# Optimization experiments

Hardware: AMD Instinct MI355X
Metric: run time of the kernel (lower is better)

The kernel has to match this reference:

```python
import jax, jax.numpy as jnp
import numpy as np

# NF4 codebook (bitsandbytes NormalFloat4 quantiles)
NF4_TABLE = jnp.array([
    -1.0, -0.6961928009986877, -0.5250730514526367, -0.39491748809814453,
    -0.28444138169288635, -0.18477343022823334, -0.09105003625154495, 0.0,
    0.07958029955625534, 0.16093020141124725, 0.24611230194568634,
    0.33791524171829224, 0.44070982933044434, 0.5626170039176941,
    0.7229568362236023, 1.0], dtype=jnp.float32)

BLOCK = 64  # bitsandbytes default quantization blocksize


def setup_inputs() -> dict:
    key = jax.random.key(0)
    ks = jax.random.split(key, 6)
    in_f, out_f, rank, n_tok = 4096, 4096, 16, 8192
    x = jax.random.normal(ks[0], (n_tok, in_f), dtype=jnp.float32)
    q_codes = jax.random.randint(ks[1], (out_f, in_f), 0, 16, dtype=jnp.int32)
    absmax = jax.random.uniform(ks[2], (out_f, in_f // BLOCK), dtype=jnp.float32) * 0.1 + 1e-3
    bias = jax.random.normal(ks[3], (out_f,), dtype=jnp.float32) * 0.02
    # kaiming-uniform-ish init for lora_down; lora_up nonzero for a meaningful test
    lora_down_w = jax.random.normal(ks[4], (rank, in_f), dtype=jnp.float32) * (1.0 / np.sqrt(in_f))
    lora_up_w = jax.random.normal(ks[5], (out_f, rank), dtype=jnp.float32) * 0.02
    alpha = jnp.array(16.0, dtype=jnp.float32)
    return {"x": x, "absmax": absmax, "bias": bias, "lora_down_w": lora_down_w,
            "lora_up_w": lora_up_w, "alpha": alpha, "q_codes": q_codes}


def reference(x, absmax, bias, lora_down_w, lora_up_w, alpha, q_codes):
    rank = lora_down_w.shape[0]
    # dequantize NF4 base weight: code lookup * per-block absmax scale
    w = NF4_TABLE[q_codes] * jnp.repeat(absmax, BLOCK, axis=1)  # [out, in]
    base = x @ w.T + bias                                       # [n_tok, out]
    # LoRA path: down [rank,in], up [out,rank], scaled by alpha/rank
    lora = (x @ lora_down_w.T) @ lora_up_w.T                    # [n_tok, out]
    return base + lora * (alpha / rank)
```

## Files before the change

### kernel.cpp

```cpp
#include <hip/hip_runtime.h>

#define IN_F 4096
#define OUT_F 4096
#define RANK 16
#define NTOK 8192
#define KP 4160
#define BK 64
#define NT (KP / BK)
#define BM 256
#define BN 256

typedef __bf16 bf16x8 __attribute__((ext_vector_type(8)));
typedef float f32x4 __attribute__((ext_vector_type(4)));

__device__ __forceinline__ unsigned short f2bf(float f) {
  unsigned int u = __float_as_uint(f);
  u += 0x7fffu + ((u >> 16) & 1u);
  return (unsigned short)(u >> 16);
}

__device__ __forceinline__ void async_ld16(const void* g, void* l) {
  __builtin_amdgcn_global_load_lds(
      (const __attribute__((address_space(1))) unsigned int*)g,
      (__attribute__((address_space(3))) unsigned int*)l, 16, 0, 0);
}

__device__ const float NF4_TAB[16] = {
    -1.0f, -0.6961928009986877f, -0.5250730514526367f, -0.39491748809814453f,
    -0.28444138169288635f, -0.18477343022823334f, -0.09105003625154495f, 0.0f,
    0.07958029955625534f, 0.16093020141124725f, 0.24611230194568634f,
    0.33791524171829224f, 0.44070982933044434f, 0.5626170039176941f,
    0.7229568362236023f, 1.0f};

__global__ __launch_bounds__(256) void k_prep_a(
    const float* __restrict__ x, const float* __restrict__ ldw,
    unsigned short* __restrict__ Ap) {
  const int tid = threadIdx.x;
  const int lane = tid & 63;
  const int w = tid >> 6;
  const int m0 = blockIdx.x * 4;

  float acc[4][4];
#pragma unroll
  for (int i = 0; i < 4; ++i)
#pragma unroll
    for (int rl = 0; rl < 4; ++rl) acc[i][rl] = 0.f;

  for (int c = 0; c < 16; ++c) {
    const int k0 = (c * 64 + lane) * 4;
    float4 xv[4];
#pragma unroll
    for (int i = 0; i < 4; ++i) {
      xv[i] = *(const float4*)&x[(size_t)(m0 + i) * IN_F + k0];
      if (w == i) {
        ushort4 s;
        s.x = f2bf(xv[i].x); s.y = f2bf(xv[i].y);
        s.z = f2bf(xv[i].z); s.w = f2bf(xv[i].w);
        *(ushort4*)&Ap[(size_t)(m0 + i) * KP + k0] = s;
      }
    }
#pragma unroll
    for (int rl = 0; rl < 4; ++rl) {
      float4 lv = *(const float4*)&ldw[(size_t)(w * 4 + rl) * IN_F + k0];
#pragma unroll
      for (int i = 0; i < 4; ++i)
        acc[i][rl] += xv[i].x * lv.x + xv[i].y * lv.y + xv[i].z * lv.z +
                      xv[i].w * lv.w;
    }
  }
#pragma unroll
  for (int i = 0; i < 4; ++i)
#pragma unroll
    for (int rl = 0; rl < 4; ++rl) {
      float v = acc[i][rl];
#pragma unroll
      for (int m = 1; m < 64; m <<= 1) v += __shfl_xor(v, m, 64);
      acc[i][rl] = v;
    }
  __shared__ float red[4][16];
  if (lane == 0) {
#pragma unroll
    for (int i = 0; i < 4; ++i)
#pragma unroll
      for (int rl = 0; rl < 4; ++rl) red[i][w * 4 + rl] = acc[i][rl];
  }
  __syncthreads();
  if (tid < 64) {
    Ap[(size_t)(m0 + (tid >> 4)) * KP + IN_F + (tid & 15)] =
        f2bf(red[tid >> 4][tid & 15]);
  } else {
    const int t2 = tid - 64;
    if (t2 < 192)
      Ap[(size_t)(m0 + t2 / 48) * KP + IN_F + 16 + (t2 % 48)] = 0;
  }
}

__global__ __launch_bounds__(256) void k_prep_b(
    const int* __restrict__ q, const float* __restrict__ amax,
    const float* __restrict__ luw, const float* __restrict__ alpha,
    unsigned short* __restrict__ Bp) {
  __shared__ float tab[16];
  const int tid = threadIdx.x;
  const int n = blockIdx.x;
  if (tid < 16) tab[tid] = NF4_TAB[tid];
  __syncthreads();
#pragma unroll
  for (int c = 0; c < 4; ++c) {
    const int k0 = (tid + 256 * c) * 4;
    int4 qv = *(const int4*)&q[(size_t)n * IN_F + k0];
    float am = amax[n * (IN_F / 64) + (k0 >> 6)];
    ushort4 s;
    s.x = f2bf(tab[qv.x] * am);
    s.y = f2bf(tab[qv.y] * am);
    s.z = f2bf(tab[qv.z] * am);
    s.w = f2bf(tab[qv.w] * am);
    *(ushort4*)&Bp[(size_t)n * KP + k0] = s;
  }
  if (tid < RANK) {
    float sc = alpha[0] * (1.0f / RANK);
    Bp[(size_t)n * KP + IN_F + tid] = f2bf(luw[n * RANK + tid] * sc);
  } else if (tid < 64) {
    Bp[(size_t)n * KP + IN_F + tid] = 0;
  }
}

__global__ __launch_bounds__(512, 1) void k_gemm(
    const unsigned short* __restrict__ Ap, const unsigned short* __restrict__ Bp,
    const float* __restrict__ bias, float* __restrict__ out) {
  __shared__ unsigned short lds[65536];
  const int tid = threadIdx.x;
  const int lane = tid & 63;
  const int w = tid >> 6;
  const int wr = w >> 2;
  const int wc = w & 3;

  const int nwg = gridDim.x * gridDim.y;
  const int flat = blockIdx.y * gridDim.x + blockIdx.x;
  const int cpx = nwg >> 3;
  const int swz = (flat & 7) * cpx + (flat >> 3);
  const int m0 = (swz / (OUT_F / BN)) * BM;
  const int n0 = (swz % (OUT_F / BN)) * BN;

  const int srow = lane >> 3;
  const int scol = (((lane & 7) ^ srow) << 3);
  const unsigned short* gA = Ap + (size_t)(m0 + (w << 4) + srow) * KP + scol;
  const unsigned short* gB = Bp + (size_t)(n0 + (w << 4) + srow) * KP + scol;
  unsigned short* const ldsw = lds + (w << 10);

  const int rdoff = ((lane & 15) << 6) + (((lane >> 4) ^ (lane & 7)) << 3);

#define STAGE2(tt, ht, cond)                                                   \
  if (cond) {                                                                  \
    const unsigned short* s_ =                                                 \
        ((ht) < 2 ? gA + (size_t)((ht) << 7) * KP                              \
                  : gB + (size_t)(((ht)-2) << 7) * KP) + (size_t)(tt)*BK;      \
    unsigned short* d_ = ldsw + ((((tt)&1) << 15) + ((ht) << 13));             \
    async_ld16(s_, d_);                                                        \
    async_ld16(s_ + (size_t)8 * KP, d_ + 512);                                 \
  }

#define LDA(bsel, mh, f, kc)                                                   \
  (*(const bf16x8*)&lds[((bsel) << 15) + (wr << 13) +                          \
                        (((mh)*64 + (f)*16) << 6) + (((kc) << 5) ^ rdoff)])
#define LDB(bsel, nh, g, kc)                                                   \
  (*(const bf16x8*)&lds[((bsel) << 15) + ((2 + (wc >> 1)) << 13) +             \
                        ((((wc & 1) * 64) + (nh)*32 + (g)*16) << 6) +          \
                        (((kc) << 5) ^ rdoff)])

#define MFMA(a, b, c) __builtin_amdgcn_mfma_f32_16x16x32_bf16((a), (b), (c), 0, 0, 0)

  STAGE2(0, 0, true) STAGE2(0, 1, true) STAGE2(0, 2, true) STAGE2(0, 3, true)
  STAGE2(1, 0, true) STAGE2(1, 1, true) STAGE2(1, 2, true) STAGE2(1, 3, true)
  asm volatile("s_waitcnt vmcnt(8)" ::: "memory");
  __builtin_amdgcn_s_barrier();

  f32x4 acc[8][4] = {};
  bf16x8 a0[4][2], a1[4][2], bq[2][2];

#pragma unroll 2
  for (int t = 0; t < NT; ++t) {
    const int bsel = t & 1;
#pragma unroll
    for (int f = 0; f < 4; ++f) {
      a0[f][0] = LDA(bsel, 0, f, 0);
      a0[f][1] = LDA(bsel, 0, f, 1);
    }
#pragma unroll
    for (int g = 0; g < 2; ++g) {
      bq[g][0] = LDB(bsel, 0, g, 0);
      bq[g][1] = LDB(bsel, 0, g, 1);
    }
    __builtin_amdgcn_s_barrier();
    asm volatile("s_waitcnt lgkmcnt(0)" ::: "memory");
    __builtin_amdgcn_sched_barrier(0);
    __builtin_amdgcn_s_setprio(1);
#pragma unroll
    for (int f = 0; f < 4; ++f)
#pragma unroll
      for (int g = 0; g < 2; ++g) {
        acc[f][g] = MFMA(a0[f][0], bq[g][0], acc[f][g]);
        acc[f][g] = MFMA(a0[f][1], bq[g][1], acc[f][g]);
      }
    __builtin_amdgcn_s_setprio(0);
    __builtin_amdgcn_s_barrier();
#pragma unroll
    for (int f = 0; f < 4; ++f) {
      a1[f][0] = LDA(bsel, 1, f, 0);
      a1[f][1] = LDA(bsel, 1, f, 1);
    }
    __builtin_amdgcn_s_barrier();
    asm volatile("s_waitcnt lgkmcnt(0)" ::: "memory");
    __builtin_amdgcn_sched_barrier(0);
    __builtin_amdgcn_s_setprio(1);
#pragma unroll
    for (int f = 0; f < 4; ++f)
#pragma unroll
      for (int g = 0; g < 2; ++g) {
        acc[4 + f][g] = MFMA(a1[f][0], bq[g][0], acc[4 + f][g]);
        acc[4 + f][g] = MFMA(a1[f][1], bq[g][1], acc[4 + f][g]);
      }
    __builtin_amdgcn_s_setprio(0);
    __builtin_amdgcn_s_barrier();
#pragma unroll
    for (int g = 0; g < 2; ++g) {
      bq[g][0] = LDB(bsel, 1, g, 0);
      bq[g][1] = LDB(bsel, 1, g, 1);
    }
    STAGE2(t + 2, 0, t + 2 < NT)
    STAGE2(t + 2, 1, t + 2 < NT)
    __builtin_amdgcn_s_barrier();
    asm volatile("s_waitcnt lgkmcnt(0)" ::: "memory");
    __builtin_amdgcn_sched_barrier(0);
    __builtin_amdgcn_s_setprio(1);
#pragma unroll
    for (int f = 0; f < 4; ++f)
#pragma unroll
      for (int g = 0; g < 2; ++g) {
        acc[4 + f][2 + g] = MFMA(a1[f][0], bq[g][0], acc[4 + f][2 + g]);
        acc[4 + f][2 + g] = MFMA(a1[f][1], bq[g][1], acc[4 + f][2 + g]);
      }
    __builtin_amdgcn_s_setprio(0);
    __builtin_amdgcn_s_barrier();
    STAGE2(t + 2, 2, t + 2 < NT)
    STAGE2(t + 2, 3, t + 2 < NT)
    __builtin_amdgcn_s_barrier();
    asm volatile("s_waitcnt lgkmcnt(0)" ::: "memory");
    __builtin_amdgcn_sched_barrier(0);
    __builtin_amdgcn_s_setprio(1);
#pragma unroll
    for (int f = 0; f < 4; ++f)
#pragma unroll
      for (int g = 0; g < 2; ++g) {
        acc[f][2 + g] = MFMA(a0[f][0], bq[g][0], acc[f][2 + g]);
        acc[f][2 + g] = MFMA(a0[f][1], bq[g][1], acc[f][2 + g]);
      }
    __builtin_amdgcn_s_setprio(0);
    if (t < NT - 2) {
      asm volatile("s_waitcnt vmcnt(8)" ::: "memory");
    } else if (t == NT - 2) {
      asm volatile("s_waitcnt vmcnt(0)" ::: "memory");
    }
    __builtin_amdgcn_s_barrier();
    __builtin_amdgcn_sched_barrier(0);
  }

  const int colL = lane & 15;
  const int rowG = lane >> 4;
#pragma unroll
  for (int nj = 0; nj < 4; ++nj) {
    const int n = n0 + wc * 64 + nj * 16 + colL;
    const float bv = bias[n];
#pragma unroll
    for (int mi = 0; mi < 8; ++mi) {
      const int mb = m0 + wr * 128 + mi * 16 + rowG * 4;
#pragma unroll
      for (int e = 0; e < 4; ++e)
        out[(size_t)(mb + e) * OUT_F + n] = acc[mi][nj][e] + bv;
    }
  }
#undef STAGE2
#undef LDA
#undef LDB
#undef MFMA
}

extern "C" void kernel_launch(void* const* d_in, const int* in_sizes, int n_in,
                              void* d_out, int out_size, void* d_ws, size_t ws_size,
                              hipStream_t stream) {
  (void)in_sizes; (void)n_in; (void)out_size; (void)ws_size;
  const float* x     = (const float*)d_in[0];
  const float* amax  = (const float*)d_in[1];
  const float* bias  = (const float*)d_in[2];
  const float* ldw   = (const float*)d_in[3];
  const float* luw   = (const float*)d_in[4];
  const float* alpha = (const float*)d_in[5];
  const int*   q     = (const int*)d_in[6];
  float* out = (float*)d_out;

  unsigned short* Ap = (unsigned short*)d_ws;
  unsigned short* Bp = Ap + (size_t)NTOK * KP;

  k_prep_a<<<NTOK / 4, 256, 0, stream>>>(x, ldw, Ap);
  k_prep_b<<<OUT_F, 256, 0, stream>>>(q, amax, luw, alpha, Bp);
  k_gemm<<<dim3(OUT_F / BN, NTOK / BM), 512, 0, stream>>>(Ap, Bp, bias, out);
}
```

Before: 344.5 us.

## Restructure GEMM main loop into register double-buffered quadrant schedule

Reorders the per-tile MFMA quadrants and keeps separate b0/b1 register fragments, so A/B fragments for the next tile are prefetched from LDS during the current tile's last quadrant. Removes most explicit lgkmcnt(0) waits and several barriers per iteration, and changes the global-load wait threshold and staging order (B halves first). The grid is also flattened to 1D with a hardcoded swizzle. This raises register pressure, and the reduced synchronisation needs the LDS buffer hazards to stay correct.

```diff
diff --git a/kernel.cpp b/kernel.cpp
--- a/kernel.cpp
+++ b/kernel.cpp
@@ -134,12 +134,10 @@
   const int wr = w >> 2;
   const int wc = w & 3;
 
-  const int nwg = gridDim.x * gridDim.y;
-  const int flat = blockIdx.y * gridDim.x + blockIdx.x;
-  const int cpx = nwg >> 3;
-  const int swz = (flat & 7) * cpx + (flat >> 3);
-  const int m0 = (swz / (OUT_F / BN)) * BM;
-  const int n0 = (swz % (OUT_F / BN)) * BN;
+  const int flat = blockIdx.x;
+  const int swz = (flat & 7) * 64 + (flat >> 3);
+  const int m0 = (swz >> 4) * BM;
+  const int n0 = (swz & 15) * BN;
 
   const int srow = lane >> 3;
   const int scol = (((lane & 7) ^ srow) << 3);
@@ -169,99 +167,110 @@
 
 #define MFMA(a, b, c) __builtin_amdgcn_mfma_f32_16x16x32_bf16((a), (b), (c), 0, 0, 0)
 
-  STAGE2(0, 0, true) STAGE2(0, 1, true) STAGE2(0, 2, true) STAGE2(0, 3, true)
-  STAGE2(1, 0, true) STAGE2(1, 1, true) STAGE2(1, 2, true) STAGE2(1, 3, true)
+  STAGE2(0, 2, true) STAGE2(0, 3, true) STAGE2(0, 0, true) STAGE2(0, 1, true)
+  STAGE2(1, 2, true) STAGE2(1, 3, true) STAGE2(1, 0, true) STAGE2(1, 1, true)
   asm volatile("s_waitcnt vmcnt(8)" ::: "memory");
   __builtin_amdgcn_s_barrier();
 
   f32x4 acc[8][4] = {};
-  bf16x8 a0[4][2], a1[4][2], bq[2][2];
+  bf16x8 a0[4][2], a1[4][2], b0[2][2], b1[2][2];
+
+#pragma unroll
+  for (int g = 0; g < 2; ++g) {
+    b0[g][0] = LDB(0, 0, g, 0);
+    b0[g][1] = LDB(0, 0, g, 1);
+  }
+#pragma unroll
+  for (int f = 0; f < 4; ++f) {
+    a0[f][0] = LDA(0, 0, f, 0);
+    a0[f][1] = LDA(0, 0, f, 1);
+  }
 
 #pragma unroll 2
   for (int t = 0; t < NT; ++t) {
     const int bsel = t & 1;
 #pragma unroll
-    for (int f = 0; f < 4; ++f) {
-      a0[f][0] = LDA(bsel, 0, f, 0);
-      a0[f][1] = LDA(bsel, 0, f, 1);
-    }
-#pragma unroll
     for (int g = 0; g < 2; ++g) {
-      bq[g][0] = LDB(bsel, 0, g, 0);
-      bq[g][1] = LDB(bsel, 0, g, 1);
-    }
-    __builtin_amdgcn_s_barrier();
-    asm volatile("s_waitcnt lgkmcnt(0)" ::: "memory");
+      b1[g][0] = LDB(bsel, 1, g, 0);
+      b1[g][1] = LDB(bsel, 1, g, 1);
+    }
+#pragma unroll
+    for (int f = 0; f < 2; ++f) {
+      a1[f][0] = LDA(bsel, 1, f, 0);
+      a1[f][1] = LDA(bsel, 1, f, 1);
+    }
     __builtin_amdgcn_sched_barrier(0);
     __builtin_amdgcn_s_setprio(1);
 #pragma unroll
     for (int f = 0; f < 4; ++f)
 #pragma unroll
       for (int g = 0; g < 2; ++g) {
-        acc[f][g] = MFMA(a0[f][0], bq[g][0], acc[f][g]);
-        acc[f][g] = MFMA(a0[f][1], bq[g][1], acc[f][g]);
+        acc[f][g] = MFMA(a0[f][0], b0[g][0], acc[f][g]);
+        acc[f][g] = MFMA(a0[f][1], b0[g][1], acc[f][g]);
       }
     __builtin_amdgcn_s_setprio(0);
     __builtin_amdgcn_s_barrier();
 #pragma unroll
-    for (int f = 0; f < 4; ++f) {
+    for (int f = 2; f < 4; ++f) {
       a1[f][0] = LDA(bsel, 1, f, 0);
       a1[f][1] = LDA(bsel, 1, f, 1);
     }
-    __builtin_amdgcn_s_barrier();
-    asm volatile("s_waitcnt lgkmcnt(0)" ::: "memory");
     __builtin_amdgcn_sched_barrier(0);
     __builtin_amdgcn_s_setprio(1);
 #pragma unroll
     for (int f = 0; f < 4; ++f)
 #pragma unroll
       for (int g = 0; g < 2; ++g) {
-        acc[4 + f][g] = MFMA(a1[f][0], bq[g][0], acc[4 + f][g]);
-        acc[4 + f][g] = MFMA(a1[f][1], bq[g][1], acc[4 + f][g]);
-      }
-    __builtin_amdgcn_s_setprio(0);
-    __builtin_amdgcn_s_barrier();
-#pragma unroll
-    for (int g = 0; g < 2; ++g) {
-      bq[g][0] = LDB(bsel, 1, g, 0);
-      bq[g][1] = LDB(bsel, 1, g, 1);
-    }
-    STAGE2(t + 2, 0, t + 2 < NT)
-    STAGE2(t + 2, 1, t + 2 < NT)
-    __builtin_amdgcn_s_barrier();
-    asm volatile("s_waitcnt lgkmcnt(0)" ::: "memory");
-    __builtin_amdgcn_sched_barrier(0);
-    __builtin_amdgcn_s_setprio(1);
-#pragma unroll
-    for (int f = 0; f < 4; ++f)
-#pragma unroll
-      for (int g = 0; g < 2; ++g) {
-        acc[4 + f][2 + g] = MFMA(a1[f][0], bq[g][0], acc[4 + f][2 + g]);
-        acc[4 + f][2 + g] = MFMA(a1[f][1], bq[g][1], acc[4 + f][2 + g]);
+        acc[f][2 + g] = MFMA(a0[f][0], b1[g][0], acc[f][2 + g]);
+        acc[f][2 + g] = MFMA(a0[f][1], b1[g][1], acc[f][2 + g]);
       }
     __builtin_amdgcn_s_setprio(0);
     __builtin_amdgcn_s_barrier();
     STAGE2(t + 2, 2, t + 2 < NT)
     STAGE2(t + 2, 3, t + 2 < NT)
-    __builtin_amdgcn_s_barrier();
-    asm volatile("s_waitcnt lgkmcnt(0)" ::: "memory");
     __builtin_amdgcn_sched_barrier(0);
     __builtin_amdgcn_s_setprio(1);
 #pragma unroll
     for (int f = 0; f < 4; ++f)
 #pragma unroll
       for (int g = 0; g < 2; ++g) {
-        acc[f][2 + g] = MFMA(a0[f][0], bq[g][0], acc[f][2 + g]);
-        acc[f][2 + g] = MFMA(a0[f][1], bq[g][1], acc[f][2 + g]);
+        acc[4 + f][2 + g] = MFMA(a1[f][0], b1[g][0], acc[4 + f][2 + g]);
+        acc[4 + f][2 + g] = MFMA(a1[f][1], b1[g][1], acc[4 + f][2 + g]);
       }
     __builtin_amdgcn_s_setprio(0);
     if (t < NT - 2) {
-      asm volatile("s_waitcnt vmcnt(8)" ::: "memory");
-    } else if (t == NT - 2) {
+      asm volatile("s_waitcnt vmcnt(4)" ::: "memory");
+    } else {
       asm volatile("s_waitcnt vmcnt(0)" ::: "memory");
     }
     __builtin_amdgcn_s_barrier();
+    if (t + 1 < NT) {
+#pragma unroll
+      for (int f = 0; f < 4; ++f) {
+        a0[f][0] = LDA(bsel ^ 1, 0, f, 0);
+        a0[f][1] = LDA(bsel ^ 1, 0, f, 1);
+      }
+    }
+    STAGE2(t + 2, 0, t + 2 < NT)
+    STAGE2(t + 2, 1, t + 2 < NT)
     __builtin_amdgcn_sched_barrier(0);
+    __builtin_amdgcn_s_setprio(1);
+#pragma unroll
+    for (int f = 0; f < 4; ++f)
+#pragma unroll
+      for (int g = 0; g < 2; ++g) {
+        acc[4 + f][g] = MFMA(a1[f][0], b0[g][0], acc[4 + f][g]);
+        acc[4 + f][g] = MFMA(a1[f][1], b0[g][1], acc[4 + f][g]);
+      }
+    __builtin_amdgcn_s_setprio(0);
+    if (t + 1 < NT) {
+#pragma unroll
+      for (int g = 0; g < 2; ++g) {
+        b0[g][0] = LDB(bsel ^ 1, 0, g, 0);
+        b0[g][1] = LDB(bsel ^ 1, 0, g, 1);
+      }
+    }
+    __builtin_amdgcn_s_barrier();
   }
 
   const int colL = lane & 15;
@@ -302,5 +311,5 @@
 
   k_prep_a<<<NTOK / 4, 256, 0, stream>>>(x, ldw, Ap);
   k_prep_b<<<OUT_F, 256, 0, stream>>>(q, amax, luw, alpha, Bp);
-  k_gemm<<<dim3(OUT_F / BN, NTOK / BM), 512, 0, stream>>>(Ap, Bp, bias, out);
-}
+  k_gemm<<<512, 512, 0, stream>>>(Ap, Bp, bias, out);
+}
```

New measurement: 343.2 us. About the same (-0.4%).
